# Performance work log

Hardware: AMD Instinct MI355X
Metric: run time of the kernel (lower is better)

## Reference

```python
import jax, jax.numpy as jnp
import numpy as np

B, N, D = 8, 1024, 512
H = 8
DH = D // H
EPS_DIST = 1e-8
EPS_LN = 1e-5


def _layer_norm(x, gamma, beta):
    mu = jnp.mean(x, axis=-1, keepdims=True)
    var = jnp.mean((x - mu) ** 2, axis=-1, keepdims=True)
    return (x - mu) * jax.lax.rsqrt(var + EPS_LN) * gamma + beta


def setup_inputs() -> dict:
    key = jax.random.key(0)
    ks = jax.random.split(key, 6)
    scale = 1.0 / np.sqrt(D)
    inp = {
        "x": jax.random.normal(ks[0], (B, N, D), dtype=jnp.float32),
        "Wq": jax.random.normal(ks[1], (D, D), dtype=jnp.float32) * scale,
        "Wk": jax.random.normal(ks[2], (D, D), dtype=jnp.float32) * scale,
        "Wv": jax.random.normal(ks[3], (D, D), dtype=jnp.float32) * scale,
        "Wo": jax.random.normal(ks[4], (D, D), dtype=jnp.float32) * scale,
        "bq": jnp.zeros((D,), jnp.float32),
        "bk": jnp.zeros((D,), jnp.float32),
        "bv": jnp.zeros((D,), jnp.float32),
        "bo": jnp.zeros((D,), jnp.float32),
        "ln1_g": jnp.ones((D,), jnp.float32),
        "ln1_b": jnp.zeros((D,), jnp.float32),
        "ln2_g": jnp.ones((D,), jnp.float32),
        "ln2_b": jnp.zeros((D,), jnp.float32),
    }
    return inp


def reference(x, Wq, bq, Wk, bk, Wv, bv, Wo, bo, ln1_g, ln1_b, ln2_g, ln2_b):
    residual = x
    h = _layer_norm(x, ln1_g, ln1_b)  # pre-norm

    def heads(t):
        # [B,N,D] -> [B,H,N,DH]
        return t.reshape(B, N, H, DH).transpose(0, 2, 1, 3)

    q = heads(h @ Wq + bq)
    k = heads(h @ Wk + bk)
    v = heads(h @ Wv + bv)

    # Euclidean pairwise distance via ||q||^2 + ||k||^2 - 2 q.k expansion
    q_sq = jnp.sum(q * q, axis=-1)[..., :, None]      # [B,H,N,1]
    k_sq = jnp.sum(k * k, axis=-1)[..., None, :]      # [B,H,1,N]
    qk = jnp.einsum("bhnd,bhmd->bhnm", q, k)          # [B,H,N,N]
    d2 = jnp.maximum(q_sq + k_sq - 2.0 * qk, 0.0)
    dist = jnp.sqrt(d2 + EPS_DIST)

    # distance -> attention score: smaller distance = higher attention
    attn = jax.nn.softmax(-dist, axis=-1)             # [B,H,N,N]

    out = jnp.einsum("bhnm,bhmd->bhnd", attn, v)      # [B,H,N,DH]
    out = out.transpose(0, 2, 1, 3).reshape(B, N, D)
    out = out @ Wo + bo

    y = residual + out
    y = _layer_norm(y, ln2_g, ln2_b)
    return y
```

## Files before the change

### kernel.cpp

```cpp
#include <hip/hip_runtime.h>
#include <math.h>

typedef __attribute__((ext_vector_type(8))) short short8;
typedef __attribute__((ext_vector_type(4))) float f32x4;
typedef __attribute__((ext_vector_type(2))) unsigned uint2v;

constexpr int B  = 8;
constexpr int N  = 1024;
constexpr int D  = 512;
constexpr int H  = 8;
constexpr int DH = 64;
constexpr int M_ROWS = 8192;
constexpr float EPS_DIST = 1e-8f;
constexpr float EPS_LN   = 1e-5f;

__device__ inline unsigned short bfbits(float f) {
    union { float f; unsigned u; } v; v.f = f;
    unsigned r = v.u + 0x7fffu + ((v.u >> 16) & 1u);
    return (unsigned short)(r >> 16);
}
__device__ inline float bf2f(unsigned short s) {
    union { unsigned u; float f; } v; v.u = ((unsigned)s) << 16; return v.f;
}

__device__ inline void async_ld16(unsigned short* lds, const unsigned short* g) {
    __builtin_amdgcn_global_load_lds(
        (const __attribute__((address_space(1))) unsigned int*)(g),
        (__attribute__((address_space(3))) unsigned int*)(lds),
        16, 0, 0);
}

__global__ __launch_bounds__(256) void prep_kernel(const float* __restrict__ Wq,
                                                   const float* __restrict__ Wk,
                                                   const float* __restrict__ Wv,
                                                   const float* __restrict__ Wo,
                                                   unsigned short* __restrict__ WtAll,
                                                   const float* __restrict__ x,
                                                   const float* __restrict__ ln1_g,
                                                   const float* __restrict__ ln1_b,
                                                   unsigned short* __restrict__ h_bf) {
    const int bxg = blockIdx.x;
    if (bxg < 256) {
        int sub = bxg >> 6;
        const float* W = sub == 0 ? Wq : sub == 1 ? Wk : sub == 2 ? Wv : Wo;
        unsigned short* Wt = WtAll + (size_t)sub * 262144;
        int t = (bxg & 63) * 256 + threadIdx.x;
        int tn = t & 127, tk = t >> 7;
        int k = tk * 4, n = tn * 4;
        float4 r0 = *(const float4*)&W[(size_t)(k + 0) * 512 + n];
        float4 r1 = *(const float4*)&W[(size_t)(k + 1) * 512 + n];
        float4 r2 = *(const float4*)&W[(size_t)(k + 2) * 512 + n];
        float4 r3 = *(const float4*)&W[(size_t)(k + 3) * 512 + n];
        ushort4 c;
        c.x = bfbits(r0.x); c.y = bfbits(r1.x); c.z = bfbits(r2.x); c.w = bfbits(r3.x);
        *(ushort4*)&Wt[(size_t)(n + 0) * 512 + k] = c;
        c.x = bfbits(r0.y); c.y = bfbits(r1.y); c.z = bfbits(r2.y); c.w = bfbits(r3.y);
        *(ushort4*)&Wt[(size_t)(n + 1) * 512 + k] = c;
        c.x = bfbits(r0.z); c.y = bfbits(r1.z); c.z = bfbits(r2.z); c.w = bfbits(r3.z);
        *(ushort4*)&Wt[(size_t)(n + 2) * 512 + k] = c;
        c.x = bfbits(r0.w); c.y = bfbits(r1.w); c.z = bfbits(r2.w); c.w = bfbits(r3.w);
        *(ushort4*)&Wt[(size_t)(n + 3) * 512 + k] = c;
    } else {
        const int w = threadIdx.x >> 6, lane = threadIdx.x & 63;
        const int row = (bxg - 256) * 4 + w;
        const float4* xr = (const float4*)(x + (size_t)row * D);
        float4 a = xr[lane], b2 = xr[lane + 64];
        float s = a.x + a.y + a.z + a.w + b2.x + b2.y + b2.z + b2.w;
        #pragma unroll
        for (int o = 1; o < 64; o <<= 1) s += __shfl_xor(s, o, 64);
        const float mu = s * (1.0f / 512.0f);
        float d0 = a.x - mu, d1 = a.y - mu, d2 = a.z - mu, d3 = a.w - mu;
        float e0 = b2.x - mu, e1 = b2.y - mu, e2 = b2.z - mu, e3 = b2.w - mu;
        float vs = d0*d0 + d1*d1 + d2*d2 + d3*d3 + e0*e0 + e1*e1 + e2*e2 + e3*e3;
        #pragma unroll
        for (int o = 1; o < 64; o <<= 1) vs += __shfl_xor(vs, o, 64);
        const float rstd = rsqrtf(vs * (1.0f / 512.0f) + EPS_LN);
        const float4* g4 = (const float4*)ln1_g;
        const float4* b4 = (const float4*)ln1_b;
        float4 ga = g4[lane], gb = g4[lane + 64];
        float4 ba = b4[lane], bb = b4[lane + 64];
        ushort4 u;
        u.x = bfbits(d0 * rstd * ga.x + ba.x);
        u.y = bfbits(d1 * rstd * ga.y + ba.y);
        u.z = bfbits(d2 * rstd * ga.z + ba.z);
        u.w = bfbits(d3 * rstd * ga.w + ba.w);
        *(ushort4*)&h_bf[(size_t)row * 512 + lane * 4] = u;
        u.x = bfbits(e0 * rstd * gb.x + bb.x);
        u.y = bfbits(e1 * rstd * gb.y + bb.y);
        u.z = bfbits(e2 * rstd * gb.z + bb.z);
        u.w = bfbits(e3 * rstd * gb.w + bb.w);
        *(ushort4*)&h_bf[(size_t)row * 512 + 256 + lane * 4] = u;
    }
}

__global__ __launch_bounds__(256) void ln2_kernel(const unsigned short* __restrict__ y0,
                                                  const float* __restrict__ res,
                                                  const float* __restrict__ gamma,
                                                  const float* __restrict__ beta,
                                                  float* __restrict__ out) {
    const int w = threadIdx.x >> 6, lane = threadIdx.x & 63;
    const int row = blockIdx.x * 4 + w;
    const ushort4* y4 = (const ushort4*)(y0 + (size_t)row * D);
    const float4*  r4 = (const float4*)(res + (size_t)row * D);
    ushort4 ya = y4[lane], yb = y4[lane + 64];
    float4  ra = r4[lane], rb = r4[lane + 64];
    float v0 = bf2f(ya.x) + ra.x, v1 = bf2f(ya.y) + ra.y;
    float v2 = bf2f(ya.z) + ra.z, v3 = bf2f(ya.w) + ra.w;
    float v4 = bf2f(yb.x) + rb.x, v5 = bf2f(yb.y) + rb.y;
    float v6 = bf2f(yb.z) + rb.z, v7 = bf2f(yb.w) + rb.w;
    float s = v0 + v1 + v2 + v3 + v4 + v5 + v6 + v7;
    #pragma unroll
    for (int o = 1; o < 64; o <<= 1) s += __shfl_xor(s, o, 64);
    const float mu = s * (1.0f / 512.0f);
    v0 -= mu; v1 -= mu; v2 -= mu; v3 -= mu;
    v4 -= mu; v5 -= mu; v6 -= mu; v7 -= mu;
    float vs = v0*v0 + v1*v1 + v2*v2 + v3*v3 + v4*v4 + v5*v5 + v6*v6 + v7*v7;
    #pragma unroll
    for (int o = 1; o < 64; o <<= 1) vs += __shfl_xor(vs, o, 64);
    const float rstd = rsqrtf(vs * (1.0f / 512.0f) + EPS_LN);
    const float4* g4 = (const float4*)gamma;
    const float4* b4 = (const float4*)beta;
    float4 ga = g4[lane], gb = g4[lane + 64];
    float4 ba = b4[lane], bb = b4[lane + 64];
    float4 o1, o2;
    o1.x = v0 * rstd * ga.x + ba.x; o1.y = v1 * rstd * ga.y + ba.y;
    o1.z = v2 * rstd * ga.z + ba.z; o1.w = v3 * rstd * ga.w + ba.w;
    o2.x = v4 * rstd * gb.x + bb.x; o2.y = v5 * rstd * gb.y + bb.y;
    o2.z = v6 * rstd * gb.z + bb.z; o2.w = v7 * rstd * gb.w + bb.w;
    float4* orow = (float4*)(out + (size_t)row * D);
    orow[lane]      = o1;
    orow[lane + 64] = o2;
}

template <int MODE, int MT>
__global__ __launch_bounds__(256) void gemm128(const unsigned short* __restrict__ A,
                                               const unsigned short* __restrict__ Wt,
                                               const float* __restrict__ bias0,
                                               const float* __restrict__ bias1,
                                               const float* __restrict__ bias2,
                                               void* __restrict__ o0,
                                               unsigned short* __restrict__ Ko,
                                               unsigned short* __restrict__ Vo,
                                               float* __restrict__ sq0,
                                               float* __restrict__ sq1) {
    constexpr int RB = M_ROWS / MT;
    constexpr int NI = MT / 32;
    constexpr int ASZ = MT * 64, BSZ = 128 * 64;
    constexpr int SMSZ = (MODE == 1) ? ((ASZ + BSZ > 18432) ? ASZ + BSZ : 18432)
                                     : (ASZ + BSZ);
    __shared__ unsigned short smem[SMSZ];
    unsigned short* As = smem;
    unsigned short* Bs = smem + ASZ;

    const int id = blockIdx.x;
    const int by = id & (RB - 1), bx = id / RB;
    const int tid = threadIdx.x;
    const int lane = tid & 63, wv = tid >> 6;
    const int quad = lane >> 4, l15 = lane & 15;
    const int row0 = by * MT, col0 = bx * 128;
    const int wm = (wv & 1) * (MT / 2), wn = (wv >> 1) * 64;

    f32x4 acc[NI][4];
    #pragma unroll
    for (int i = 0; i < NI; ++i)
        #pragma unroll
        for (int j = 0; j < 4; ++j) acc[i][j] = (f32x4){0.f, 0.f, 0.f, 0.f};

    const unsigned short* Ag = A  + (size_t)row0 * 512;
    const unsigned short* Bg = Wt + (size_t)col0 * 512;

    for (int k0 = 0; k0 < 512; k0 += 64) {
        __syncthreads();
        #pragma unroll
        for (int c = 0; c < ASZ / 2048; ++c) {
            int fu = c * 2048 + tid * 8;
            int r = fu >> 6, ko = fu & 63;
            async_ld16(As + fu, Ag + (size_t)r * 512 + k0 + ko);
        }
        #pragma unroll
        for (int c = 0; c < BSZ / 2048; ++c) {
            int fu = c * 2048 + tid * 8;
            int r = fu >> 6, ko = fu & 63;
            async_ld16(Bs + fu, Bg + (size_t)r * 512 + k0 + ko);
        }
        __syncthreads();

        #pragma unroll
        for (int ks = 0; ks < 2; ++ks) {
            short8 af[NI], bf[4];
            #pragma unroll
            for (int i = 0; i < NI; ++i)
                af[i] = *(const short8*)&As[(wm + i * 16 + l15) * 64 + ks * 32 + quad * 8];
            #pragma unroll
            for (int j = 0; j < 4; ++j)
                bf[j] = *(const short8*)&Bs[(wn + j * 16 + l15) * 64 + ks * 32 + quad * 8];
            #pragma unroll
            for (int i = 0; i < NI; ++i)
                #pragma unroll
                for (int j = 0; j < 4; ++j)
                    acc[i][j] = __builtin_amdgcn_mfma_f32_16x16x32_bf16(af[i], bf[j], acc[i][j], 0, 0, 0);
        }
    }

    if (MODE == 0) {
        unsigned short* C = (unsigned short*)o0;
        #pragma unroll
        for (int i = 0; i < NI; ++i)
            #pragma unroll
            for (int j = 0; j < 4; ++j) {
                int col = col0 + wn + j * 16 + l15;
                float bv = bias0[col];
                #pragma unroll
                for (int r = 0; r < 4; ++r) {
                    int row = row0 + wm + i * 16 + quad * 4 + r;
                    C[(size_t)row * 512 + col] = bfbits(acc[i][j][r] + bv);
                }
            }
    } else {
        const int colg = col0 + wn;
        const int seg = colg >> 9;
        const int hh = (colg & 511) >> 6;
        const float* bias = seg == 0 ? bias0 : seg == 1 ? bias1 : bias2;

        __syncthreads();
        unsigned short* T = smem + wv * 4608;

        if (seg < 2) {
            unsigned short* dst = seg == 0 ? (unsigned short*)o0 : Ko;
            float* sq = seg == 0 ? sq0 : sq1;
            #pragma unroll
            for (int i = 0; i < NI; ++i) {
                const int m0 = row0 + wm + i * 16 + quad * 4;
                float ss[4] = {0.f, 0.f, 0.f, 0.f};
                #pragma unroll
                for (int j = 0; j < 4; ++j) {
                    float bvj = bias[hh * 64 + j * 16 + l15];
                    #pragma unroll
                    for (int r = 0; r < 4; ++r) {
                        float v = acc[i][j][r] + bvj;
                        unsigned short ub = bfbits(v);
                        float vr = bf2f(ub);
                        ss[r] += vr * vr;
                        T[(i * 16 + quad * 4 + r) * 72 + j * 16 + l15] = ub;
                    }
                }
                #pragma unroll
                for (int r = 0; r < 4; ++r) {
                    float s = ss[r];
                    s += __shfl_xor(s, 1, 64);
                    s += __shfl_xor(s, 2, 64);
                    s += __shfl_xor(s, 4, 64);
                    s += __shfl_xor(s, 8, 64);
                    if (l15 == 0) {
                        int m = m0 + r;
                        sq[(size_t)((m >> 10) * 8 + hh) * 1024 + (m & 1023)] = s;
                    }
                }
            }
            const int b_ = (row0 + wm) >> 10;
            const int nbase = (row0 + wm) & 1023;
            unsigned short* Dg = dst + ((size_t)((b_ * 8 + hh) * 1024 + nbase)) * 64;
            #pragma unroll
            for (int it = 0; it < 8; ++it) {
                int ml = it * 8 + (lane >> 3);
                int dl = (lane & 7) * 8;
                uint4 v = *(const uint4*)&T[ml * 72 + dl];
                *(uint4*)&Dg[(size_t)ml * 64 + dl] = v;
            }
        } else {
            #pragma unroll
            for (int i = 0; i < NI; ++i)
                #pragma unroll
                for (int j = 0; j < 4; ++j) {
                    float bvj = bias[hh * 64 + j * 16 + l15];
                    ushort4 pk;
                    pk.x = bfbits(acc[i][j][0] + bvj);
                    pk.y = bfbits(acc[i][j][1] + bvj);
                    pk.z = bfbits(acc[i][j][2] + bvj);
                    pk.w = bfbits(acc[i][j][3] + bvj);
                    *(ushort4*)&T[(j * 16 + l15) * 72 + i * 16 + quad * 4] = pk;
                }
            const int b_ = (row0 + wm) >> 10;
            const int nbase = (row0 + wm) & 1023;
            unsigned short* Vg = Vo + ((size_t)((b_ * 8 + hh) * 64)) * 1024 + nbase;
            #pragma unroll
            for (int it = 0; it < 8; ++it) {
                int dl = it * 8 + (lane >> 3);
                int nl = (lane & 7) * 8;
                uint4 v = *(const uint4*)&T[dl * 72 + nl];
                *(uint4*)&Vg[(size_t)dl * 1024 + nl] = v;
            }
        }
    }
}

__global__ __launch_bounds__(256, 2) void attn_kernel(const unsigned short* __restrict__ Q,
                                                      const unsigned short* __restrict__ K,
                                                      const unsigned short* __restrict__ Vt,
                                                      const float* __restrict__ qsq,
                                                      const float* __restrict__ ksq,
                                                      unsigned short* __restrict__ O) {
    __shared__ unsigned short smem[2 * 4096 + 2 * 4096 + 256];
    unsigned short* KsB = smem;
    unsigned short* VsB = smem + 8192;
    float* ksq_s = (float*)(smem + 16384);

    const int id = blockIdx.x;
    const int bh = id & 63, qb = id >> 6;
    const int q0 = qb * 128;
    const int tid = threadIdx.x;
    const int lane = tid & 63, w = tid >> 6;
    const int quad = lane >> 4, l15 = lane & 15;
    const int b_ = bh >> 3, h_ = bh & 7;

    const unsigned short* Qb = Q  + (size_t)bh * N * DH;
    const unsigned short* Kb = K  + (size_t)bh * N * DH;
    const unsigned short* Vb = Vt + (size_t)bh * DH * N;

    short8 qf[2][2];
    #pragma unroll
    for (int qh = 0; qh < 2; ++qh) {
        const unsigned short* qp = Qb + (size_t)(q0 + w * 32 + qh * 16 + l15) * 64 + quad * 8;
        qf[qh][0] = *(const short8*)qp;
        qf[qh][1] = *(const short8*)(qp + 32);
        unsigned* qw = (unsigned*)&qf[qh][0];
        #pragma unroll
        for (int j = 0; j < 8; ++j) qw[j] = (qw[j] ^ 0x80008000u) + 0x00800080u;
    }
    float qe[2];
    qe[0] = qsq[bh * N + q0 + w * 32 + l15] + EPS_DIST;
    qe[1] = qsq[bh * N + q0 + w * 32 + 16 + l15] + EPS_DIST;

    const short8 onesf = {0x3F80, 0x3F80, 0x3F80, 0x3F80, 0x3F80, 0x3F80, 0x3F80, 0x3F80};

    f32x4 oacc[2][4];
    f32x4 dsum[2];
    #pragma unroll
    for (int qh = 0; qh < 2; ++qh) {
        dsum[qh] = (f32x4){0.f, 0.f, 0.f, 0.f};
        #pragma unroll
        for (int dt = 0; dt < 4; ++dt) oacc[qh][dt] = (f32x4){0.f, 0.f, 0.f, 0.f};
    }

    const int srow = tid >> 3;
    const int scol = ((tid & 7) * 8) ^ ((srow & 7) << 3);

    #pragma unroll
    for (int c = 0; c < 2; ++c) {
        const int e = c * 2048 + tid * 8;
        const int row = srow + c * 32;
        async_ld16(KsB + e, Kb + (size_t)row * 64 + scol);
        async_ld16(VsB + e, Vb + (size_t)row * N + scol);
    }
    if (tid < 64) ksq_s[tid] = ksq[bh * N + tid];
    __syncthreads();

    for (int kt = 0; kt < 16; ++kt) {
        const int cur = kt & 1;
        float ksreg = 0.f;
        if (kt < 15) {
            const int t64 = (kt + 1) * 64;
            #pragma unroll
            for (int c = 0; c < 2; ++c) {
                const int e = (cur ^ 1) * 4096 + c * 2048 + tid * 8;
                const int row = (c * 2048 + tid * 8) >> 6;
                const int cg = ((tid & 7) * 8) ^ ((row & 7) << 3);
                async_ld16(KsB + e, Kb + (size_t)(t64 + row) * 64 + cg);
                async_ld16(VsB + e, Vb + (size_t)row * N + t64 + cg);
            }
            if (tid < 64) ksreg = ksq[bh * N + t64 + tid];
        }

        #pragma unroll
        for (int kc = 0; kc < 2; ++kc) {
            unsigned Wp[2][2][2];
            #pragma unroll
            for (int kh = 0; kh < 2; ++kh) {
                const int kb = kc * 2 + kh;
                const int krow = kb * 16 + l15;
                const int ksw = (krow & 7) << 3;
                const unsigned short* kbase = KsB + cur * 4096 + krow * 64;
                short8 kf0 = *(const short8*)&kbase[(quad * 8) ^ ksw];
                short8 kf1 = *(const short8*)&kbase[(32 + quad * 8) ^ ksw];
                f32x4 ks2 = *(const f32x4*)&ksq_s[cur * 64 + kb * 16 + quad * 4];
                #pragma unroll
                for (int qh = 0; qh < 2; ++qh) {
                    f32x4 sa;
                    #pragma unroll
                    for (int r = 0; r < 4; ++r) sa[r] = ks2[r] + qe[qh];
                    sa = __builtin_amdgcn_mfma_f32_16x16x32_bf16(kf0, qf[qh][0], sa, 0, 0, 0);
                    sa = __builtin_amdgcn_mfma_f32_16x16x32_bf16(kf1, qf[qh][1], sa, 0, 0, 0);
                    float pr[4];
                    #pragma unroll
                    for (int r = 0; r < 4; ++r) {
                        float d2 = fmaxf(sa[r], EPS_DIST);
                        pr[r] = __expf(-__builtin_amdgcn_sqrtf(d2));
                    }
                    union { float f; unsigned u; } u0, u1, u2, u3;
                    u0.f = pr[0]; u1.f = pr[1]; u2.f = pr[2]; u3.f = pr[3];
                    Wp[qh][kh][0] = __builtin_amdgcn_perm(u1.u, u0.u, 0x07060302u);
                    Wp[qh][kh][1] = __builtin_amdgcn_perm(u3.u, u2.u, 0x07060302u);
                }
            }

            short8 vf[4];
            #pragma unroll
            for (int dt = 0; dt < 4; ++dt) {
                const int vrow = dt * 16 + l15;
                vf[dt] = *(const short8*)&VsB[cur * 4096 + vrow * 64 +
                                              ((kc * 32 + quad * 8) ^ ((vrow & 7) << 3))];
            }

            #pragma unroll
            for (int qh = 0; qh < 2; ++qh) {
                uint2v ya = __builtin_amdgcn_permlane32_swap(Wp[qh][0][0], Wp[qh][1][0], false, false);
                uint2v za = __builtin_amdgcn_permlane16_swap(ya.x, ya.y, false, false);
                uint2v yb = __builtin_amdgcn_permlane32_swap(Wp[qh][0][1], Wp[qh][1][1], false, false);
                uint2v zb = __builtin_amdgcn_permlane16_swap(yb.x, yb.y, false, false);
                union { unsigned wds[4]; short8 s; } pu;
                pu.wds[0] = za.x; pu.wds[1] = zb.x; pu.wds[2] = za.y; pu.wds[3] = zb.y;
                short8 pf = pu.s;
                dsum[qh] = __builtin_amdgcn_mfma_f32_16x16x32_bf16(pf, onesf, dsum[qh], 0, 0, 0);
                #pragma unroll
                for (int dt = 0; dt < 4; ++dt)
                    oacc[qh][dt] = __builtin_amdgcn_mfma_f32_16x16x32_bf16(pf, vf[dt], oacc[qh][dt], 0, 0, 0);
            }
        }

        if (kt < 15 && tid < 64) ksq_s[(cur ^ 1) * 64 + tid] = ksreg;
        __syncthreads();
    }

    unsigned short* T3 = smem + w * 2304;
    #pragma unroll
    for (int qh = 0; qh < 2; ++qh) {
        f32x4 rv;
        #pragma unroll
        for (int r = 0; r < 4; ++r) rv[r] = __builtin_amdgcn_rcpf(dsum[qh][r]);
        #pragma unroll
        for (int dt = 0; dt < 4; ++dt)
            #pragma unroll
            for (int r = 0; r < 4; ++r)
                T3[(qh * 16 + quad * 4 + r) * 72 + dt * 16 + l15] =
                    bfbits(oacc[qh][dt][r] * rv[r]);
    }
    unsigned short* Og = O + ((size_t)(b_ * N + q0 + w * 32) * D) + h_ * DH;
    #pragma unroll
    for (int it = 0; it < 4; ++it) {
        int ml = it * 8 + (lane >> 3);
        int dl = (lane & 7) * 8;
        uint4 v = *(const uint4*)&T3[ml * 72 + dl];
        *(uint4*)&Og[(size_t)ml * D + dl] = v;
    }
}

extern "C" void kernel_launch(void* const* d_in, const int* in_sizes, int n_in,
                              void* d_out, int out_size, void* d_ws, size_t ws_size,
                              hipStream_t stream) {
    const float* x     = (const float*)d_in[0];
    const float* Wq    = (const float*)d_in[1];
    const float* Wk    = (const float*)d_in[2];
    const float* Wv    = (const float*)d_in[3];
    const float* Wo    = (const float*)d_in[4];
    const float* bq    = (const float*)d_in[5];
    const float* bk    = (const float*)d_in[6];
    const float* bv    = (const float*)d_in[7];
    const float* bo    = (const float*)d_in[8];
    const float* ln1_g = (const float*)d_in[9];
    const float* ln1_b = (const float*)d_in[10];
    const float* ln2_g = (const float*)d_in[11];
    const float* ln2_b = (const float*)d_in[12];
    float* out = (float*)d_out;

    unsigned short* WtAll = (unsigned short*)d_ws;
    unsigned short* h_bf  = WtAll + 4 * 262144;
    unsigned short* Qb    = h_bf + 4194304;
    unsigned short* Kb    = Qb + 4194304;
    unsigned short* Vtg   = Kb + 4194304;
    unsigned short* Ob    = Vtg + 4194304;
    unsigned short* Y0    = Ob + 4194304;
    float* qsq = (float*)(Y0 + 4194304);
    float* ksq = qsq + 65536;

    prep_kernel<<<256 + M_ROWS / 4, 256, 0, stream>>>(Wq, Wk, Wv, Wo, WtAll,
                                                      x, ln1_g, ln1_b, h_bf);

    gemm128<1, 128><<<768, 256, 0, stream>>>(h_bf, WtAll, bq, bk, bv,
                                             Qb, Kb, Vtg, qsq, ksq);

    attn_kernel<<<512, 256, 0, stream>>>(Qb, Kb, Vtg, qsq, ksq, Ob);

    gemm128<0, 64><<<512, 256, 0, stream>>>(Ob, WtAll + 3 * 262144, bo,
                                            nullptr, nullptr, Y0,
                                            nullptr, nullptr, nullptr, nullptr);

    ln2_kernel<<<M_ROWS / 4, 256, 0, stream>>>(Y0, x, ln2_g, ln2_b, out);
}
```

Baseline: 174.0 us.

## Fuse output projection with residual and LayerNorm; swizzle GEMM LDS tiles

Replaces the separate output-projection GEMM and ln2 kernel with one kernel that computes 32 full rows of the projection, adds bias and residual, and applies LayerNorm in registers. This drops the bf16 Y0 round trip and one launch, and keeps the output in fp32 before the norm. The GEMM shared-memory tiles get an XOR swizzle to cut bank conflicts. It also changes the thread mapping in the weight transpose and the row index in the attention K/V prefetch. The fused kernel launches only 256 blocks and stages a full 512x64 B tile per k-step, which may limit occupancy.

```diff
diff --git a/kernel.cpp b/kernel.cpp
--- a/kernel.cpp
+++ b/kernel.cpp
@@ -45,7 +45,7 @@
         const float* W = sub == 0 ? Wq : sub == 1 ? Wk : sub == 2 ? Wv : Wo;
         unsigned short* Wt = WtAll + (size_t)sub * 262144;
         int t = (bxg & 63) * 256 + threadIdx.x;
-        int tn = t & 127, tk = t >> 7;
+        int tk = t & 127, tn = t >> 7;
         int k = tk * 4, n = tn * 4;
         float4 r0 = *(const float4*)&W[(size_t)(k + 0) * 512 + n];
         float4 r1 = *(const float4*)&W[(size_t)(k + 1) * 512 + n];
@@ -93,45 +93,6 @@
     }
 }
 
-__global__ __launch_bounds__(256) void ln2_kernel(const unsigned short* __restrict__ y0,
-                                                  const float* __restrict__ res,
-                                                  const float* __restrict__ gamma,
-                                                  const float* __restrict__ beta,
-                                                  float* __restrict__ out) {
-    const int w = threadIdx.x >> 6, lane = threadIdx.x & 63;
-    const int row = blockIdx.x * 4 + w;
-    const ushort4* y4 = (const ushort4*)(y0 + (size_t)row * D);
-    const float4*  r4 = (const float4*)(res + (size_t)row * D);
-    ushort4 ya = y4[lane], yb = y4[lane + 64];
-    float4  ra = r4[lane], rb = r4[lane + 64];
-    float v0 = bf2f(ya.x) + ra.x, v1 = bf2f(ya.y) + ra.y;
-    float v2 = bf2f(ya.z) + ra.z, v3 = bf2f(ya.w) + ra.w;
-    float v4 = bf2f(yb.x) + rb.x, v5 = bf2f(yb.y) + rb.y;
-    float v6 = bf2f(yb.z) + rb.z, v7 = bf2f(yb.w) + rb.w;
-    float s = v0 + v1 + v2 + v3 + v4 + v5 + v6 + v7;
-    #pragma unroll
-    for (int o = 1; o < 64; o <<= 1) s += __shfl_xor(s, o, 64);
-    const float mu = s * (1.0f / 512.0f);
-    v0 -= mu; v1 -= mu; v2 -= mu; v3 -= mu;
-    v4 -= mu; v5 -= mu; v6 -= mu; v7 -= mu;
-    float vs = v0*v0 + v1*v1 + v2*v2 + v3*v3 + v4*v4 + v5*v5 + v6*v6 + v7*v7;
-    #pragma unroll
-    for (int o = 1; o < 64; o <<= 1) vs += __shfl_xor(vs, o, 64);
-    const float rstd = rsqrtf(vs * (1.0f / 512.0f) + EPS_LN);
-    const float4* g4 = (const float4*)gamma;
-    const float4* b4 = (const float4*)beta;
-    float4 ga = g4[lane], gb = g4[lane + 64];
-    float4 ba = b4[lane], bb = b4[lane + 64];
-    float4 o1, o2;
-    o1.x = v0 * rstd * ga.x + ba.x; o1.y = v1 * rstd * ga.y + ba.y;
-    o1.z = v2 * rstd * ga.z + ba.z; o1.w = v3 * rstd * ga.w + ba.w;
-    o2.x = v4 * rstd * gb.x + bb.x; o2.y = v5 * rstd * gb.y + bb.y;
-    o2.z = v6 * rstd * gb.z + bb.z; o2.w = v7 * rstd * gb.w + bb.w;
-    float4* orow = (float4*)(out + (size_t)row * D);
-    orow[lane]      = o1;
-    orow[lane + 64] = o2;
-}
-
 template <int MODE, int MT>
 __global__ __launch_bounds__(256) void gemm128(const unsigned short* __restrict__ A,
                                                const unsigned short* __restrict__ Wt,
@@ -159,6 +120,7 @@
     const int quad = lane >> 4, l15 = lane & 15;
     const int row0 = by * MT, col0 = bx * 128;
     const int wm = (wv & 1) * (MT / 2), wn = (wv >> 1) * 64;
+    const int fsw = (l15 & 7) << 3;
 
     f32x4 acc[NI][4];
     #pragma unroll
@@ -175,13 +137,13 @@
         for (int c = 0; c < ASZ / 2048; ++c) {
             int fu = c * 2048 + tid * 8;
             int r = fu >> 6, ko = fu & 63;
-            async_ld16(As + fu, Ag + (size_t)r * 512 + k0 + ko);
+            async_ld16(As + fu, Ag + (size_t)r * 512 + k0 + (ko ^ ((r & 7) << 3)));
         }
         #pragma unroll
         for (int c = 0; c < BSZ / 2048; ++c) {
             int fu = c * 2048 + tid * 8;
             int r = fu >> 6, ko = fu & 63;
-            async_ld16(Bs + fu, Bg + (size_t)r * 512 + k0 + ko);
+            async_ld16(Bs + fu, Bg + (size_t)r * 512 + k0 + (ko ^ ((r & 7) << 3)));
         }
         __syncthreads();
 
@@ -190,10 +152,12 @@
             short8 af[NI], bf[4];
             #pragma unroll
             for (int i = 0; i < NI; ++i)
-                af[i] = *(const short8*)&As[(wm + i * 16 + l15) * 64 + ks * 32 + quad * 8];
+                af[i] = *(const short8*)&As[(wm + i * 16 + l15) * 64 +
+                                            ((ks * 32 + quad * 8) ^ fsw)];
             #pragma unroll
             for (int j = 0; j < 4; ++j)
-                bf[j] = *(const short8*)&Bs[(wn + j * 16 + l15) * 64 + ks * 32 + quad * 8];
+                bf[j] = *(const short8*)&Bs[(wn + j * 16 + l15) * 64 +
+                                            ((ks * 32 + quad * 8) ^ fsw)];
             #pragma unroll
             for (int i = 0; i < NI; ++i)
                 #pragma unroll
@@ -294,6 +258,163 @@
     }
 }
 
+__global__ __launch_bounds__(256) void projln_kernel(const unsigned short* __restrict__ A,
+                                                     const unsigned short* __restrict__ Wt,
+                                                     const float* __restrict__ bo,
+                                                     const float* __restrict__ x,
+                                                     const float* __restrict__ gamma,
+                                                     const float* __restrict__ beta,
+                                                     float* __restrict__ out) {
+    __shared__ unsigned short smem[2048 + 32768];
+    __shared__ float st[128];
+    unsigned short* As = smem;
+    unsigned short* Bs = smem + 2048;
+
+    const int tid = threadIdx.x;
+    const int lane = tid & 63, w = tid >> 6;
+    const int quad = lane >> 4, l15 = lane & 15;
+    const int rows0 = blockIdx.x * 32;
+    const int fsw = (l15 & 7) << 3;
+
+    f32x4 acc[2][8];
+    #pragma unroll
+    for (int i = 0; i < 2; ++i)
+        #pragma unroll
+        for (int j = 0; j < 8; ++j) acc[i][j] = (f32x4){0.f, 0.f, 0.f, 0.f};
+
+    const unsigned short* Ag = A + (size_t)rows0 * 512;
+    const int sr = tid >> 3;
+    const int sko = (tid & 7) * 8;
+
+    for (int k0 = 0; k0 < 512; k0 += 64) {
+        __syncthreads();
+        async_ld16(As + tid * 8,
+                   Ag + (size_t)sr * 512 + k0 + (sko ^ ((sr & 7) << 3)));
+        #pragma unroll
+        for (int c = 0; c < 16; ++c) {
+            int fu = c * 2048 + tid * 8;
+            int r = c * 32 + sr;
+            async_ld16(Bs + fu,
+                       Wt + (size_t)r * 512 + k0 + (sko ^ ((r & 7) << 3)));
+        }
+        __syncthreads();
+
+        #pragma unroll
+        for (int ks = 0; ks < 2; ++ks) {
+            short8 af[2], bf[8];
+            #pragma unroll
+            for (int i = 0; i < 2; ++i)
+                af[i] = *(const short8*)&As[(i * 16 + l15) * 64 +
+                                            ((ks * 32 + quad * 8) ^ fsw)];
+            #pragma unroll
+            for (int j = 0; j < 8; ++j)
+                bf[j] = *(const short8*)&Bs[(w * 128 + j * 16 + l15) * 64 +
+                                            ((ks * 32 + quad * 8) ^ fsw)];
+            #pragma unroll
+            for (int i = 0; i < 2; ++i)
+                #pragma unroll
+                for (int j = 0; j < 8; ++j)
+                    acc[i][j] = __builtin_amdgcn_mfma_f32_16x16x32_bf16(af[i], bf[j], acc[i][j], 0, 0, 0);
+        }
+    }
+
+    float s1[2][4] = {{0.f, 0.f, 0.f, 0.f}, {0.f, 0.f, 0.f, 0.f}};
+    #pragma unroll
+    for (int i = 0; i < 2; ++i)
+        #pragma unroll
+        for (int j = 0; j < 8; ++j) {
+            const int colj = w * 128 + j * 16 + l15;
+            const float bvj = bo[colj];
+            #pragma unroll
+            for (int r = 0; r < 4; ++r) {
+                const int row = i * 16 + quad * 4 + r;
+                float y = acc[i][j][r] + bvj +
+                          x[(size_t)(rows0 + row) * 512 + colj];
+                acc[i][j][r] = y;
+                s1[i][r] += y;
+            }
+        }
+    #pragma unroll
+    for (int i = 0; i < 2; ++i)
+        #pragma unroll
+        for (int r = 0; r < 4; ++r) {
+            s1[i][r] += __shfl_xor(s1[i][r], 1, 64);
+            s1[i][r] += __shfl_xor(s1[i][r], 2, 64);
+            s1[i][r] += __shfl_xor(s1[i][r], 4, 64);
+            s1[i][r] += __shfl_xor(s1[i][r], 8, 64);
+        }
+    if (l15 == 0) {
+        #pragma unroll
+        for (int i = 0; i < 2; ++i)
+            #pragma unroll
+            for (int r = 0; r < 4; ++r)
+                st[w * 32 + i * 16 + quad * 4 + r] = s1[i][r];
+    }
+    __syncthreads();
+    float mu[2][4];
+    #pragma unroll
+    for (int i = 0; i < 2; ++i)
+        #pragma unroll
+        for (int r = 0; r < 4; ++r) {
+            int row = i * 16 + quad * 4 + r;
+            mu[i][r] = (st[row] + st[32 + row] + st[64 + row] + st[96 + row]) *
+                       (1.0f / 512.0f);
+        }
+    __syncthreads();
+
+    float s2[2][4] = {{0.f, 0.f, 0.f, 0.f}, {0.f, 0.f, 0.f, 0.f}};
+    #pragma unroll
+    for (int i = 0; i < 2; ++i)
+        #pragma unroll
+        for (int j = 0; j < 8; ++j)
+            #pragma unroll
+            for (int r = 0; r < 4; ++r) {
+                float d = acc[i][j][r] - mu[i][r];
+                s2[i][r] += d * d;
+            }
+    #pragma unroll
+    for (int i = 0; i < 2; ++i)
+        #pragma unroll
+        for (int r = 0; r < 4; ++r) {
+            s2[i][r] += __shfl_xor(s2[i][r], 1, 64);
+            s2[i][r] += __shfl_xor(s2[i][r], 2, 64);
+            s2[i][r] += __shfl_xor(s2[i][r], 4, 64);
+            s2[i][r] += __shfl_xor(s2[i][r], 8, 64);
+        }
+    if (l15 == 0) {
+        #pragma unroll
+        for (int i = 0; i < 2; ++i)
+            #pragma unroll
+            for (int r = 0; r < 4; ++r)
+                st[w * 32 + i * 16 + quad * 4 + r] = s2[i][r];
+    }
+    __syncthreads();
+    float rs[2][4];
+    #pragma unroll
+    for (int i = 0; i < 2; ++i)
+        #pragma unroll
+        for (int r = 0; r < 4; ++r) {
+            int row = i * 16 + quad * 4 + r;
+            float var = (st[row] + st[32 + row] + st[64 + row] + st[96 + row]) *
+                        (1.0f / 512.0f);
+            rs[i][r] = rsqrtf(var + EPS_LN);
+        }
+
+    #pragma unroll
+    for (int i = 0; i < 2; ++i)
+        #pragma unroll
+        for (int j = 0; j < 8; ++j) {
+            const int colj = w * 128 + j * 16 + l15;
+            const float gl = gamma[colj], bl = beta[colj];
+            #pragma unroll
+            for (int r = 0; r < 4; ++r) {
+                const int row = i * 16 + quad * 4 + r;
+                out[(size_t)(rows0 + row) * 512 + colj] =
+                    (acc[i][j][r] - mu[i][r]) * rs[i][r] * gl + bl;
+            }
+        }
+}
+
 __global__ __launch_bounds__(256, 2) void attn_kernel(const unsigned short* __restrict__ Q,
                                                       const unsigned short* __restrict__ K,
                                                       const unsigned short* __restrict__ Vt,
@@ -363,7 +484,7 @@
             #pragma unroll
             for (int c = 0; c < 2; ++c) {
                 const int e = (cur ^ 1) * 4096 + c * 2048 + tid * 8;
-                const int row = (c * 2048 + tid * 8) >> 6;
+                const int row = srow + c * 32;
                 const int cg = ((tid & 7) * 8) ^ ((row & 7) << 3);
                 async_ld16(KsB + e, Kb + (size_t)(t64 + row) * 64 + cg);
                 async_ld16(VsB + e, Vb + (size_t)row * N + t64 + cg);
@@ -478,8 +599,7 @@
     unsigned short* Kb    = Qb + 4194304;
     unsigned short* Vtg   = Kb + 4194304;
     unsigned short* Ob    = Vtg + 4194304;
-    unsigned short* Y0    = Ob + 4194304;
-    float* qsq = (float*)(Y0 + 4194304);
+    float* qsq = (float*)(Ob + 4194304);
     float* ksq = qsq + 65536;
 
     prep_kernel<<<256 + M_ROWS / 4, 256, 0, stream>>>(Wq, Wk, Wv, Wo, WtAll,
@@ -490,9 +610,6 @@
 
     attn_kernel<<<512, 256, 0, stream>>>(Qb, Kb, Vtg, qsq, ksq, Ob);
 
-    gemm128<0, 64><<<512, 256, 0, stream>>>(Ob, WtAll + 3 * 262144, bo,
-                                            nullptr, nullptr, Y0,
-                                            nullptr, nullptr, nullptr, nullptr);
-
-    ln2_kernel<<<M_ROWS / 4, 256, 0, stream>>>(Y0, x, ln2_g, ln2_b, out);
-}
+    projln_kernel<<<256, 256, 0, stream>>>(Ob, WtAll + 3 * 262144, bo,
+                                           x, ln2_g, ln2_b, out);
+}
```

New measurement: 171.4 us (median of 2 runs). Within noise of the previous version (-1.5%).
